# Kernel tuning notes

Hardware: AMD Instinct MI355X
Metric: run time of the kernel (lower is better)

## Reference

```python
import jax, jax.numpy as jnp
import numpy as np

N_NODES = 50000
N_EDGES = 800000
N_RELS = 32
D_IN = 64
D_OUT = 64


def setup_inputs() -> dict:
    key = jax.random.key(0)
    k_feat, k_w, k_src, k_dst, k_et = jax.random.split(key, 5)
    feat = jax.random.normal(k_feat, (N_NODES, D_IN), dtype=jnp.float32)
    weight = jax.random.normal(k_w, (N_RELS, D_IN, D_OUT), dtype=jnp.float32) * 0.05
    src = jax.random.randint(k_src, (N_EDGES,), 0, N_NODES, dtype=jnp.int32)
    dst = jax.random.randint(k_dst, (N_EDGES,), 0, N_NODES, dtype=jnp.int32)
    etypes = jax.random.randint(k_et, (N_EDGES,), 0, N_RELS, dtype=jnp.int32)
    # per-relation edge counts (unused by the unsorted math, kept for API fidelity)
    E_per_rel = jnp.bincount(etypes, length=N_RELS)
    return {"feat": feat, "weight": weight, "src": src, "dst": dst,
            "etypes": etypes, "E_per_rel": E_per_rel}


def reference(feat, weight, src, dst, etypes, E_per_rel):
    # out[d] = sum_{e: dst[e]==d} feat[src[e]] @ weight[etypes[e]]
    # Since the per-edge matmul is linear in feat, we first segment-sum the
    # gathered source features by (dst, etype), then apply each relation's
    # weight once. This avoids materializing an [E, D_IN, D_OUT] tensor.
    N = feat.shape[0]
    R, D_in, D_out = weight.shape
    gathered = feat[src]                                   # [E, D_in]
    seg = dst.astype(jnp.int32) * R + etypes.astype(jnp.int32)  # [E]
    per_node_rel = jax.ops.segment_sum(gathered, seg, num_segments=N * R)
    per_node_rel = per_node_rel.reshape(N, R, D_in)        # [N, R, D_in]
    out = jnp.einsum('nri,rio->no', per_node_rel, weight)  # [N, D_out]
    return out
```

## Files before the change

### kernel.cpp

```cpp
#include <hip/hip_runtime.h>
#include <hip/hip_bf16.h>

#define N_NODES 50000
#define N_EDGES 800000
#define N_RELS  32
#define D       64
#define TILE_M  128
#define NBKT    196
#define EPB     2048
#define NEBLK   ((N_EDGES + EPB - 1) / EPB)

typedef _Float16 half8 __attribute__((ext_vector_type(8)));
typedef float    f32x4 __attribute__((ext_vector_type(4)));

#define OFF_RELHIST 0u
#define OFF_BKTHIST 128u
#define OFF_RELCUR  1024u
#define OFF_BKTCUR  1152u
#define OFF_ROFF    1936u
#define OFF_TB      2080u
#define OFF_BKTOFF  2224u
#define OFF_DSTOFF  3072u
#define OFF_RELSRC  203776u
#define OFF_J2POS   3403776u
#define OFF_WT      6603776u
#define OFF_FEATH   6865920u
#define OFF_Y_FULL  13265920u
#define OFF_Y_BASE  6865920u
#define WS_FULL     115665920u
#define WS_BASE     109265920u

__global__ __launch_bounds__(256) void rgcn_edge_atomic(
    const float* __restrict__ feat, const float* __restrict__ weight,
    const int* __restrict__ src, const int* __restrict__ dst,
    const int* __restrict__ et, float* __restrict__ out, int nquads)
{
    const int tid  = blockIdx.x * blockDim.x + threadIdx.x;
    const int wave = tid >> 6, lane = tid & 63;
    const int grp = lane >> 4, lg = lane & 15;
    const int wave_stride = (gridDim.x * blockDim.x) >> 6;
    for (int q = wave; q < nquads; q += wave_stride) {
        const int e = q * 4 + grp;
        const int s = src[e], d = dst[e], r = et[e];
        const float* w = weight + (size_t)r * D * D + lg * 4;
        float ax = 0.f, ay = 0.f, az = 0.f, aw = 0.f;
        #pragma unroll
        for (int i4 = 0; i4 < D / 4; ++i4) {
            const float4 f  = *reinterpret_cast<const float4*>(feat + (size_t)s * D + i4 * 4);
            const float4 w0 = *reinterpret_cast<const float4*>(w + (i4 * 4 + 0) * D);
            const float4 w1 = *reinterpret_cast<const float4*>(w + (i4 * 4 + 1) * D);
            const float4 w2 = *reinterpret_cast<const float4*>(w + (i4 * 4 + 2) * D);
            const float4 w3 = *reinterpret_cast<const float4*>(w + (i4 * 4 + 3) * D);
            ax += f.x*w0.x; ay += f.x*w0.y; az += f.x*w0.z; aw += f.x*w0.w;
            ax += f.y*w1.x; ay += f.y*w1.y; az += f.y*w1.z; aw += f.y*w1.w;
            ax += f.z*w2.x; ay += f.z*w2.y; az += f.z*w2.z; aw += f.z*w2.w;
            ax += f.w*w3.x; ay += f.w*w3.y; az += f.w*w3.z; aw += f.w*w3.w;
        }
        float* orow = out + (size_t)d * D + lg * 4;
        atomicAdd(orow + 0, ax); atomicAdd(orow + 1, ay);
        atomicAdd(orow + 2, az); atomicAdd(orow + 3, aw);
    }
}

__global__ __launch_bounds__(256) void kPre(const float* __restrict__ w,
                                            _Float16* __restrict__ wT,
                                            const float* __restrict__ feat,
                                            _Float16* __restrict__ featH)
{
    const int t = threadIdx.x;
    if (blockIdx.x < N_RELS) {
        const int r = blockIdx.x;
        #pragma unroll
        for (int i = 0; i < 16; ++i) {
            int oidx = i * 256 + t;
            int o = oidx >> 6, k = oidx & 63;
            wT[(size_t)r * 4096 + oidx] = (_Float16)w[(size_t)r * 4096 + k * 64 + o];
        }
    } else {
        const int base = ((blockIdx.x - N_RELS) * 256 + t) * 8;
        if (base >= N_NODES * D) return;
        float4 f0 = *reinterpret_cast<const float4*>(feat + base);
        float4 f1 = *reinterpret_cast<const float4*>(feat + base + 4);
        half8 h;
        h[0]=(_Float16)f0.x; h[1]=(_Float16)f0.y; h[2]=(_Float16)f0.z; h[3]=(_Float16)f0.w;
        h[4]=(_Float16)f1.x; h[5]=(_Float16)f1.y; h[6]=(_Float16)f1.z; h[7]=(_Float16)f1.w;
        *reinterpret_cast<half8*>(featH + base) = h;
    }
}

__global__ __launch_bounds__(256) void kA_hist(const int* __restrict__ et,
                                               const int* __restrict__ dst,
                                               int* __restrict__ relhist,
                                               int* __restrict__ bkthist)
{
    __shared__ int lh[N_RELS];
    __shared__ int lb[NBKT];
    const int t = threadIdx.x;
    if (t < N_RELS) lh[t] = 0;
    if (t < NBKT)   lb[t] = 0;
    __syncthreads();
    const int base = blockIdx.x * EPB + t * 8;
    #pragma unroll
    for (int i = 0; i < 8; ++i) {
        int e = base + i;
        if (e < N_EDGES) {
            atomicAdd(&lh[et[e]], 1);
            atomicAdd(&lb[dst[e] >> 8], 1);
        }
    }
    __syncthreads();
    if (t < N_RELS && lh[t]) atomicAdd(&relhist[t], lh[t]);
    if (t < NBKT   && lb[t]) atomicAdd(&bkthist[t], lb[t]);
}

__global__ __launch_bounds__(256) void kB_scan(const int* __restrict__ relhist,
                                               const int* __restrict__ bkthist,
                                               int* __restrict__ roff,
                                               int* __restrict__ relcur,
                                               int* __restrict__ tb,
                                               int* __restrict__ bktoff,
                                               int* __restrict__ bktcur,
                                               int* __restrict__ dst_off)
{
    __shared__ int s[256];
    const int t = threadIdx.x;
    int v = (t < N_RELS) ? relhist[t] : 0;
    s[t] = v; __syncthreads();
    #pragma unroll
    for (int off = 1; off < 32; off <<= 1) {
        int u = (t >= off && t < N_RELS) ? s[t - off] : 0;
        __syncthreads(); s[t] += u; __syncthreads();
    }
    if (t < N_RELS) { int ex = s[t] - v; roff[t] = ex; relcur[t] = ex; }
    if (t == N_RELS - 1) roff[N_RELS] = s[t];
    __syncthreads();
    int w = (v + TILE_M - 1) / TILE_M;
    s[t] = (t < N_RELS) ? w : 0; __syncthreads();
    #pragma unroll
    for (int off = 1; off < 32; off <<= 1) {
        int u = (t >= off && t < N_RELS) ? s[t - off] : 0;
        __syncthreads(); s[t] += u; __syncthreads();
    }
    if (t < N_RELS) tb[t] = s[t] - w;
    if (t == N_RELS - 1) tb[N_RELS] = s[t];
    __syncthreads();
    int v2 = (t < NBKT) ? bkthist[t] : 0;
    s[t] = v2; __syncthreads();
    #pragma unroll
    for (int off = 1; off < 256; off <<= 1) {
        int u = (t >= off) ? s[t - off] : 0;
        __syncthreads(); s[t] += u; __syncthreads();
    }
    if (t < NBKT) { int ex = s[t] - v2; bktoff[t] = ex; bktcur[t] = ex; }
    if (t == NBKT - 1) bktoff[NBKT] = s[t];
    if (t == 0) dst_off[N_NODES] = N_EDGES;
}

__global__ __launch_bounds__(256) void kC_scatter(const int* __restrict__ src,
                                                  const int* __restrict__ dst,
                                                  const int* __restrict__ et,
                                                  int* __restrict__ relcur,
                                                  int* __restrict__ bktcur,
                                                  int* __restrict__ relsrc,
                                                  int* __restrict__ bucketed)
{
    __shared__ int lh[N_RELS],  lbase[N_RELS];
    __shared__ int lb[NBKT],    lbase2[NBKT];
    const int t = threadIdx.x;
    if (t < N_RELS) lh[t] = 0;
    if (t < NBKT)   lb[t] = 0;
    __syncthreads();
    const int base = blockIdx.x * EPB + t * 8;
    int r_[8], b_[8], s_[8], d_[8], sl[8], sl2[8];
    #pragma unroll
    for (int i = 0; i < 8; ++i) {
        int e = base + i;
        if (e < N_EDGES) {
            r_[i] = et[e]; s_[i] = src[e]; d_[i] = dst[e];
            b_[i] = d_[i] >> 8;
            sl[i]  = atomicAdd(&lh[r_[i]], 1);
            sl2[i] = atomicAdd(&lb[b_[i]], 1);
        }
    }
    __syncthreads();
    if (t < N_RELS && lh[t]) lbase[t]  = atomicAdd(&relcur[t], lh[t]);
    if (t < NBKT   && lb[t]) lbase2[t] = atomicAdd(&bktcur[t], lb[t]);
    __syncthreads();
    #pragma unroll
    for (int i = 0; i < 8; ++i) {
        int e = base + i;
        if (e < N_EDGES) {
            int j = lbase[r_[i]] + sl[i];
            relsrc[j] = s_[i];
            bucketed[lbase2[b_[i]] + sl2[i]] = ((d_[i] & 255) << 20) | j;
        }
    }
}

__global__ __launch_bounds__(256) void kD_csr(const int* __restrict__ bucketed,
                                              const int* __restrict__ bktoff,
                                              int* __restrict__ j2pos,
                                              int* __restrict__ dst_off)
{
    __shared__ int hist[256];
    __shared__ int s[256];
    const int b = blockIdx.x, t = threadIdx.x;
    const int lo = bktoff[b], hi = bktoff[b + 1];
    hist[t] = 0; __syncthreads();
    for (int p = lo + t; p < hi; p += 256)
        atomicAdd(&hist[bucketed[p] >> 20], 1);
    __syncthreads();
    int v = hist[t];
    s[t] = v; __syncthreads();
    #pragma unroll
    for (int off = 1; off < 256; off <<= 1) {
        int u = (t >= off) ? s[t - off] : 0;
        __syncthreads(); s[t] += u; __syncthreads();
    }
    int ex = lo + s[t] - v;
    int n = b * 256 + t;
    if (n < N_NODES) dst_off[n] = ex;
    hist[t] = ex;
    __syncthreads();
    for (int p = lo + t; p < hi; p += 256) {
        int key = bucketed[p];
        int pos = atomicAdd(&hist[key >> 20], 1);
        j2pos[key & 0xFFFFF] = pos;
    }
}

template <bool USE_H>
__global__ __launch_bounds__(256) void k4_gemm(const float* __restrict__ feat,
                                               const _Float16* __restrict__ featH,
                                               const _Float16* __restrict__ wT,
                                               const int* __restrict__ relsrc,
                                               const int* __restrict__ j2pos,
                                               const int* __restrict__ roff,
                                               const int* __restrict__ tb,
                                               _Float16* __restrict__ Y)
{
    __shared__ _Float16 aT[TILE_M * 64];
    __shared__ _Float16 wL[64 * 64];
    __shared__ int      ypos[TILE_M];
    const int b = blockIdx.x, t = threadIdx.x;

    int r = -1, ti = 0, t0 = 0;
    #pragma unroll
    for (int q = 0; q < N_RELS; ++q) {
        int t1 = tb[q + 1];
        if (b >= t0 && b < t1) { r = q; ti = b - t0; }
        t0 = t1;
    }
    if (r < 0) return;
    const int segend  = roff[r + 1];
    const int rowbase = roff[r] + ti * TILE_M;

    if (t < TILE_M) {
        const int j = rowbase + t;
        const bool ok = (j < segend);
        const int sidx = ok ? relsrc[j] : 0;
        ypos[t] = ok ? j2pos[j] : 0;
        if (USE_H) {
            const half8* hrow = reinterpret_cast<const half8*>(featH + (size_t)sidx * 64);
            #pragma unroll
            for (int c = 0; c < 4; ++c) {
                half8 h0 = hrow[c * 2 + 0];
                half8 h1 = hrow[c * 2 + 1];
                int base = t * 128 + c * 32;
                int a0 = (base)      ^ ((t & 7) << 4);
                int a1 = (base + 16) ^ ((t & 7) << 4);
                *reinterpret_cast<half8*>(reinterpret_cast<char*>(aT) + a0) = h0;
                *reinterpret_cast<half8*>(reinterpret_cast<char*>(aT) + a1) = h1;
            }
        } else {
            const float4* frow = reinterpret_cast<const float4*>(feat + (size_t)sidx * 64);
            #pragma unroll
            for (int c = 0; c < 4; ++c) {
                float4 f0 = frow[c*4+0], f1 = frow[c*4+1], f2 = frow[c*4+2], f3 = frow[c*4+3];
                half8 h0, h1;
                h0[0]=(_Float16)f0.x; h0[1]=(_Float16)f0.y; h0[2]=(_Float16)f0.z; h0[3]=(_Float16)f0.w;
                h0[4]=(_Float16)f1.x; h0[5]=(_Float16)f1.y; h0[6]=(_Float16)f1.z; h0[7]=(_Float16)f1.w;
                h1[0]=(_Float16)f2.x; h1[1]=(_Float16)f2.y; h1[2]=(_Float16)f2.z; h1[3]=(_Float16)f2.w;
                h1[4]=(_Float16)f3.x; h1[5]=(_Float16)f3.y; h1[6]=(_Float16)f3.z; h1[7]=(_Float16)f3.w;
                int base = t * 128 + c * 32;
                int a0 = (base)      ^ ((t & 7) << 4);
                int a1 = (base + 16) ^ ((t & 7) << 4);
                *reinterpret_cast<half8*>(reinterpret_cast<char*>(aT) + a0) = h0;
                *reinterpret_cast<half8*>(reinterpret_cast<char*>(aT) + a1) = h1;
            }
        }
    } else {
        const _Float16* wsrc = wT + (size_t)r * 4096;
        const int tt = t - 128;
        #pragma unroll
        for (int it = 0; it < 4; ++it) {
            int L8 = it * 128 + tt;
            int o = L8 >> 3, kcol = (L8 & 7) * 8;
            int baddr = (o * 128 + kcol * 2) ^ ((o & 7) << 4);
            *reinterpret_cast<half8*>(reinterpret_cast<char*>(wL) + baddr) =
                *reinterpret_cast<const half8*>(wsrc + L8 * 8);
        }
    }
    __syncthreads();

    const int wid = t >> 6, l = t & 63;
    const int lrow = l & 15, lkb = l >> 4;
    f32x4 acc[2][4] = {};
    #pragma unroll
    for (int ks = 0; ks < 2; ++ks) {
        half8 af[2], bfr[4];
        #pragma unroll
        for (int rt = 0; rt < 2; ++rt) {
            int row = wid * 32 + rt * 16 + lrow;
            int baddr = (row * 128 + ks * 64 + lkb * 16) ^ ((row & 7) << 4);
            af[rt] = *reinterpret_cast<const half8*>(reinterpret_cast<const char*>(aT) + baddr);
        }
        #pragma unroll
        for (int ct = 0; ct < 4; ++ct) {
            int n = ct * 16 + lrow;
            int baddr = (n * 128 + ks * 64 + lkb * 16) ^ ((n & 7) << 4);
            bfr[ct] = *reinterpret_cast<const half8*>(reinterpret_cast<const char*>(wL) + baddr);
        }
        #pragma unroll
        for (int rt = 0; rt < 2; ++rt)
            #pragma unroll
            for (int ct = 0; ct < 4; ++ct)
                acc[rt][ct] = __builtin_amdgcn_mfma_f32_16x16x32_f16(af[rt], bfr[ct], acc[rt][ct], 0, 0, 0);
    }
    #pragma unroll
    for (int rt = 0; rt < 2; ++rt) {
        int lrow0 = wid * 32 + rt * 16 + (l >> 4) * 4;
        #pragma unroll
        for (int reg = 0; reg < 4; ++reg) {
            int lr = lrow0 + reg;
            if (rowbase + lr < segend) {
                size_t yrow = (size_t)ypos[lr] * 64;
                #pragma unroll
                for (int ct = 0; ct < 4; ++ct)
                    Y[yrow + ct * 16 + lrow] = (_Float16)acc[rt][ct][reg];
            }
        }
    }
}

__global__ __launch_bounds__(256) void k5_reduce(const _Float16* __restrict__ Y,
                                                 const int* __restrict__ dst_off,
                                                 float* __restrict__ out)
{
    const int wid = threadIdx.x >> 6, l = threadIdx.x & 63;
    const int n = blockIdx.x * 4 + wid;
    if (n >= N_NODES) return;
    const int p0 = dst_off[n], p1 = dst_off[n + 1];
    float acc = 0.f;
    int p = p0;
    for (; p + 4 <= p1; p += 4) {
        acc += (float)Y[(size_t)(p+0) * 64 + l] + (float)Y[(size_t)(p+1) * 64 + l]
             + (float)Y[(size_t)(p+2) * 64 + l] + (float)Y[(size_t)(p+3) * 64 + l];
    }
    for (; p < p1; ++p)
        acc += (float)Y[(size_t)p * 64 + l];
    out[(size_t)n * 64 + l] = acc;
}

extern "C" void kernel_launch(void* const* d_in, const int* in_sizes, int n_in,
                              void* d_out, int out_size, void* d_ws, size_t ws_size,
                              hipStream_t stream) {
    const float* feat   = (const float*)d_in[0];
    const float* weight = (const float*)d_in[1];
    const int*   src    = (const int*)d_in[2];
    const int*   dst    = (const int*)d_in[3];
    const int*   et     = (const int*)d_in[4];
    float*       out    = (float*)d_out;

    if (ws_size < (size_t)WS_BASE) {
        hipMemsetAsync(d_out, 0, (size_t)out_size * sizeof(float), stream);
        hipLaunchKernelGGL(rgcn_edge_atomic, dim3(4096), dim3(256), 0, stream,
                           feat, weight, src, dst, et, out, N_EDGES / 4);
        return;
    }
    const bool use_h = (ws_size >= (size_t)WS_FULL);

    char* ws = (char*)d_ws;
    int*       relhist  = (int*)(ws + OFF_RELHIST);
    int*       bkthist  = (int*)(ws + OFF_BKTHIST);
    int*       relcur   = (int*)(ws + OFF_RELCUR);
    int*       bktcur   = (int*)(ws + OFF_BKTCUR);
    int*       roff     = (int*)(ws + OFF_ROFF);
    int*       tb       = (int*)(ws + OFF_TB);
    int*       bktoff   = (int*)(ws + OFF_BKTOFF);
    int*       dst_off  = (int*)(ws + OFF_DSTOFF);
    int*       relsrc   = (int*)(ws + OFF_RELSRC);
    int*       j2pos    = (int*)(ws + OFF_J2POS);
    _Float16*  wT       = (_Float16*)(ws + OFF_WT);
    _Float16*  featH    = (_Float16*)(ws + OFF_FEATH);
    _Float16*  Y        = (_Float16*)(ws + (use_h ? OFF_Y_FULL : OFF_Y_BASE));
    int*       bucketed = (int*)Y;

    hipMemsetAsync(ws, 0, 912, stream);

    const int pre_blocks = use_h ? (N_RELS + (N_NODES * D / 8 + 255) / 256) : N_RELS;
    hipLaunchKernelGGL(kPre,       dim3(pre_blocks), dim3(256), 0, stream, weight, wT, feat, featH);
    hipLaunchKernelGGL(kA_hist,    dim3(NEBLK),  dim3(256), 0, stream, et, dst, relhist, bkthist);
    hipLaunchKernelGGL(kB_scan,    dim3(1),      dim3(256), 0, stream, relhist, bkthist, roff, relcur, tb, bktoff, bktcur, dst_off);
    hipLaunchKernelGGL(kC_scatter, dim3(NEBLK),  dim3(256), 0, stream, src, dst, et, relcur, bktcur, relsrc, bucketed);
    hipLaunchKernelGGL(kD_csr,     dim3(NBKT),   dim3(256), 0, stream, bucketed, bktoff, j2pos, dst_off);
    const int max_tiles = N_EDGES / TILE_M + N_RELS;
    if (use_h)
        hipLaunchKernelGGL((k4_gemm<true>),  dim3(max_tiles), dim3(256), 0, stream, feat, featH, wT, relsrc, j2pos, roff, tb, Y);
    else
        hipLaunchKernelGGL((k4_gemm<false>), dim3(max_tiles), dim3(256), 0, stream, feat, featH, wT, relsrc, j2pos, roff, tb, Y);
    hipLaunchKernelGGL(k5_reduce,  dim3((N_NODES + 3) / 4), dim3(256), 0, stream, Y, dst_off, out);
}
```

Before: 119.5 us.

## Fuse histogram with preprocessing, vectorize reduce, split gemm tile loads across all threads

Measured after the change: 130.4 us. +9.2%, slower.

```diff
diff --git a/kernel.cpp b/kernel.cpp
--- a/kernel.cpp
+++ b/kernel.cpp
@@ -7,8 +7,10 @@
 #define D       64
 #define TILE_M  128
 #define NBKT    196
-#define EPB     2048
+#define EPB     1024
+#define EPT     4
 #define NEBLK   ((N_EDGES + EPB - 1) / EPB)
+#define FEATH_BLKS ((N_NODES * D / 8 + 255) / 256)
 
 typedef _Float16 half8 __attribute__((ext_vector_type(8)));
 typedef float    f32x4 __attribute__((ext_vector_type(4)));
@@ -62,14 +64,41 @@
     }
 }
 
-__global__ __launch_bounds__(256) void kPre(const float* __restrict__ w,
-                                            _Float16* __restrict__ wT,
-                                            const float* __restrict__ feat,
-                                            _Float16* __restrict__ featH)
-{
-    const int t = threadIdx.x;
-    if (blockIdx.x < N_RELS) {
-        const int r = blockIdx.x;
+__global__ __launch_bounds__(256) void kZ_zero(int* __restrict__ h)
+{
+    if (threadIdx.x < 228) h[threadIdx.x] = 0;
+}
+
+__global__ __launch_bounds__(256) void kA_fused(const int* __restrict__ et,
+                                                const int* __restrict__ dst,
+                                                int* __restrict__ relhist,
+                                                int* __restrict__ bkthist,
+                                                const float* __restrict__ w,
+                                                _Float16* __restrict__ wT,
+                                                const float* __restrict__ feat,
+                                                _Float16* __restrict__ featH)
+{
+    __shared__ int lh[N_RELS];
+    __shared__ int lb[NBKT];
+    const int t = threadIdx.x, b = blockIdx.x;
+    if (b < NEBLK) {
+        if (t < N_RELS) lh[t] = 0;
+        if (t < NBKT)   lb[t] = 0;
+        __syncthreads();
+        const int base = b * EPB + t * EPT;
+        #pragma unroll
+        for (int i = 0; i < EPT; ++i) {
+            int e = base + i;
+            if (e < N_EDGES) {
+                atomicAdd(&lh[et[e]], 1);
+                atomicAdd(&lb[dst[e] >> 8], 1);
+            }
+        }
+        __syncthreads();
+        if (t < N_RELS && lh[t]) atomicAdd(&relhist[t], lh[t]);
+        if (t < NBKT   && lb[t]) atomicAdd(&bkthist[t], lb[t]);
+    } else if (b < NEBLK + N_RELS) {
+        const int r = b - NEBLK;
         #pragma unroll
         for (int i = 0; i < 16; ++i) {
             int oidx = i * 256 + t;
@@ -77,40 +106,15 @@
             wT[(size_t)r * 4096 + oidx] = (_Float16)w[(size_t)r * 4096 + k * 64 + o];
         }
     } else {
-        const int base = ((blockIdx.x - N_RELS) * 256 + t) * 8;
-        if (base >= N_NODES * D) return;
-        float4 f0 = *reinterpret_cast<const float4*>(feat + base);
-        float4 f1 = *reinterpret_cast<const float4*>(feat + base + 4);
+        const int base2 = ((b - NEBLK - N_RELS) * 256 + t) * 8;
+        if (base2 >= N_NODES * D) return;
+        float4 f0 = *reinterpret_cast<const float4*>(feat + base2);
+        float4 f1 = *reinterpret_cast<const float4*>(feat + base2 + 4);
         half8 h;
         h[0]=(_Float16)f0.x; h[1]=(_Float16)f0.y; h[2]=(_Float16)f0.z; h[3]=(_Float16)f0.w;
         h[4]=(_Float16)f1.x; h[5]=(_Float16)f1.y; h[6]=(_Float16)f1.z; h[7]=(_Float16)f1.w;
-        *reinterpret_cast<half8*>(featH + base) = h;
-    }
-}
-
-__global__ __launch_bounds__(256) void kA_hist(const int* __restrict__ et,
-                                               const int* __restrict__ dst,
-                                               int* __restrict__ relhist,
-                                               int* __restrict__ bkthist)
-{
-    __shared__ int lh[N_RELS];
-    __shared__ int lb[NBKT];
-    const int t = threadIdx.x;
-    if (t < N_RELS) lh[t] = 0;
-    if (t < NBKT)   lb[t] = 0;
-    __syncthreads();
-    const int base = blockIdx.x * EPB + t * 8;
-    #pragma unroll
-    for (int i = 0; i < 8; ++i) {
-        int e = base + i;
-        if (e < N_EDGES) {
-            atomicAdd(&lh[et[e]], 1);
-            atomicAdd(&lb[dst[e] >> 8], 1);
-        }
-    }
-    __syncthreads();
-    if (t < N_RELS && lh[t]) atomicAdd(&relhist[t], lh[t]);
-    if (t < NBKT   && lb[t]) atomicAdd(&bkthist[t], lb[t]);
+        *reinterpret_cast<half8*>(featH + base2) = h;
+    }
 }
 
 __global__ __launch_bounds__(256) void kB_scan(const int* __restrict__ relhist,
@@ -170,10 +174,10 @@
     if (t < N_RELS) lh[t] = 0;
     if (t < NBKT)   lb[t] = 0;
     __syncthreads();
-    const int base = blockIdx.x * EPB + t * 8;
-    int r_[8], b_[8], s_[8], d_[8], sl[8], sl2[8];
-    #pragma unroll
-    for (int i = 0; i < 8; ++i) {
+    const int base = blockIdx.x * EPB + t * EPT;
+    int r_[EPT], b_[EPT], s_[EPT], d_[EPT], sl[EPT], sl2[EPT];
+    #pragma unroll
+    for (int i = 0; i < EPT; ++i) {
         int e = base + i;
         if (e < N_EDGES) {
             r_[i] = et[e]; s_[i] = src[e]; d_[i] = dst[e];
@@ -187,7 +191,7 @@
     if (t < NBKT   && lb[t]) lbase2[t] = atomicAdd(&bktcur[t], lb[t]);
     __syncthreads();
     #pragma unroll
-    for (int i = 0; i < 8; ++i) {
+    for (int i = 0; i < EPT; ++i) {
         int e = base + i;
         if (e < N_EDGES) {
             int j = lbase[r_[i]] + sl[i];
@@ -255,46 +259,44 @@
     const int segend  = roff[r + 1];
     const int rowbase = roff[r] + ti * TILE_M;
 
-    if (t < TILE_M) {
-        const int j = rowbase + t;
+    {
+        const int row = t & 127, hh = t >> 7;
+        const int j = rowbase + row;
         const bool ok = (j < segend);
         const int sidx = ok ? relsrc[j] : 0;
-        ypos[t] = ok ? j2pos[j] : 0;
+        if (hh == 0) ypos[row] = ok ? j2pos[j] : 0;
+        const int sw = (row & 7) << 4;
         if (USE_H) {
             const half8* hrow = reinterpret_cast<const half8*>(featH + (size_t)sidx * 64);
             #pragma unroll
-            for (int c = 0; c < 4; ++c) {
+            for (int cc = 0; cc < 2; ++cc) {
+                int c = hh * 2 + cc;
                 half8 h0 = hrow[c * 2 + 0];
                 half8 h1 = hrow[c * 2 + 1];
-                int base = t * 128 + c * 32;
-                int a0 = (base)      ^ ((t & 7) << 4);
-                int a1 = (base + 16) ^ ((t & 7) << 4);
-                *reinterpret_cast<half8*>(reinterpret_cast<char*>(aT) + a0) = h0;
-                *reinterpret_cast<half8*>(reinterpret_cast<char*>(aT) + a1) = h1;
+                int base = row * 128 + c * 32;
+                *reinterpret_cast<half8*>(reinterpret_cast<char*>(aT) + ((base)      ^ sw)) = h0;
+                *reinterpret_cast<half8*>(reinterpret_cast<char*>(aT) + ((base + 16) ^ sw)) = h1;
             }
         } else {
             const float4* frow = reinterpret_cast<const float4*>(feat + (size_t)sidx * 64);
             #pragma unroll
-            for (int c = 0; c < 4; ++c) {
+            for (int cc = 0; cc < 2; ++cc) {
+                int c = hh * 2 + cc;
                 float4 f0 = frow[c*4+0], f1 = frow[c*4+1], f2 = frow[c*4+2], f3 = frow[c*4+3];
                 half8 h0, h1;
                 h0[0]=(_Float16)f0.x; h0[1]=(_Float16)f0.y; h0[2]=(_Float16)f0.z; h0[3]=(_Float16)f0.w;
                 h0[4]=(_Float16)f1.x; h0[5]=(_Float16)f1.y; h0[6]=(_Float16)f1.z; h0[7]=(_Float16)f1.w;
                 h1[0]=(_Float16)f2.x; h1[1]=(_Float16)f2.y; h1[2]=(_Float16)f2.z; h1[3]=(_Float16)f2.w;
                 h1[4]=(_Float16)f3.x; h1[5]=(_Float16)f3.y; h1[6]=(_Float16)f3.z; h1[7]=(_Float16)f3.w;
-                int base = t * 128 + c * 32;
-                int a0 = (base)      ^ ((t & 7) << 4);
-                int a1 = (base + 16) ^ ((t & 7) << 4);
-                *reinterpret_cast<half8*>(reinterpret_cast<char*>(aT) + a0) = h0;
-                *reinterpret_cast<half8*>(reinterpret_cast<char*>(aT) + a1) = h1;
+                int base = row * 128 + c * 32;
+                *reinterpret_cast<half8*>(reinterpret_cast<char*>(aT) + ((base)      ^ sw)) = h0;
+                *reinterpret_cast<half8*>(reinterpret_cast<char*>(aT) + ((base + 16) ^ sw)) = h1;
             }
         }
-    } else {
         const _Float16* wsrc = wT + (size_t)r * 4096;
-        const int tt = t - 128;
-        #pragma unroll
-        for (int it = 0; it < 4; ++it) {
-            int L8 = it * 128 + tt;
+        #pragma unroll
+        for (int it = 0; it < 2; ++it) {
+            int L8 = it * 256 + t;
             int o = L8 >> 3, kcol = (L8 & 7) * 8;
             int baddr = (o * 128 + kcol * 2) ^ ((o & 7) << 4);
             *reinterpret_cast<half8*>(reinterpret_cast<char*>(wL) + baddr) =
@@ -351,15 +353,29 @@
     const int n = blockIdx.x * 4 + wid;
     if (n >= N_NODES) return;
     const int p0 = dst_off[n], p1 = dst_off[n + 1];
-    float acc = 0.f;
-    int p = p0;
-    for (; p + 4 <= p1; p += 4) {
-        acc += (float)Y[(size_t)(p+0) * 64 + l] + (float)Y[(size_t)(p+1) * 64 + l]
-             + (float)Y[(size_t)(p+2) * 64 + l] + (float)Y[(size_t)(p+3) * 64 + l];
-    }
-    for (; p < p1; ++p)
-        acc += (float)Y[(size_t)p * 64 + l];
-    out[(size_t)n * 64 + l] = acc;
+    const int rg = l >> 3;
+    const int cg = l & 7;
+    float a[8] = {0,0,0,0,0,0,0,0};
+    for (int p = p0; p < p1; p += 8) {
+        int row = p + rg;
+        if (row < p1) {
+            half8 v = *reinterpret_cast<const half8*>(Y + (size_t)row * 64 + cg * 8);
+            #pragma unroll
+            for (int i = 0; i < 8; ++i) a[i] += (float)v[i];
+        }
+    }
+    #pragma unroll
+    for (int m = 8; m < 64; m <<= 1)
+        #pragma unroll
+        for (int i = 0; i < 8; ++i)
+            a[i] += __shfl_xor(a[i], m, 64);
+    if (rg == 0) {
+        float* orow = out + (size_t)n * 64 + cg * 8;
+        f32x4 v0 = {a[0], a[1], a[2], a[3]};
+        f32x4 v1 = {a[4], a[5], a[6], a[7]};
+        *reinterpret_cast<f32x4*>(orow)     = v0;
+        *reinterpret_cast<f32x4*>(orow + 4) = v1;
+    }
 }
 
 extern "C" void kernel_launch(void* const* d_in, const int* in_sizes, int n_in,
@@ -396,18 +412,17 @@
     _Float16*  Y        = (_Float16*)(ws + (use_h ? OFF_Y_FULL : OFF_Y_BASE));
     int*       bucketed = (int*)Y;
 
-    hipMemsetAsync(ws, 0, 912, stream);
-
-    const int pre_blocks = use_h ? (N_RELS + (N_NODES * D / 8 + 255) / 256) : N_RELS;
-    hipLaunchKernelGGL(kPre,       dim3(pre_blocks), dim3(256), 0, stream, weight, wT, feat, featH);
-    hipLaunchKernelGGL(kA_hist,    dim3(NEBLK),  dim3(256), 0, stream, et, dst, relhist, bkthist);
-    hipLaunchKernelGGL(kB_scan,    dim3(1),      dim3(256), 0, stream, relhist, bkthist, roff, relcur, tb, bktoff, bktcur, dst_off);
-    hipLaunchKernelGGL(kC_scatter, dim3(NEBLK),  dim3(256), 0, stream, src, dst, et, relcur, bktcur, relsrc, bucketed);
-    hipLaunchKernelGGL(kD_csr,     dim3(NBKT),   dim3(256), 0, stream, bucketed, bktoff, j2pos, dst_off);
+    hipLaunchKernelGGL(kZ_zero,   dim3(1), dim3(256), 0, stream, (int*)ws);
+    const int ka_blocks = NEBLK + N_RELS + (use_h ? FEATH_BLKS : 0);
+    hipLaunchKernelGGL(kA_fused,  dim3(ka_blocks), dim3(256), 0, stream,
+                       et, dst, relhist, bkthist, weight, wT, feat, featH);
+    hipLaunchKernelGGL(kB_scan,   dim3(1),     dim3(256), 0, stream, relhist, bkthist, roff, relcur, tb, bktoff, bktcur, dst_off);
+    hipLaunchKernelGGL(kC_scatter,dim3(NEBLK), dim3(256), 0, stream, src, dst, et, relcur, bktcur, relsrc, bucketed);
+    hipLaunchKernelGGL(kD_csr,    dim3(NBKT),  dim3(256), 0, stream, bucketed, bktoff, j2pos, dst_off);
     const int max_tiles = N_EDGES / TILE_M + N_RELS;
     if (use_h)
         hipLaunchKernelGGL((k4_gemm<true>),  dim3(max_tiles), dim3(256), 0, stream, feat, featH, wT, relsrc, j2pos, roff, tb, Y);
     else
         hipLaunchKernelGGL((k4_gemm<false>), dim3(max_tiles), dim3(256), 0, stream, feat, featH, wT, relsrc, j2pos, roff, tb, Y);
-    hipLaunchKernelGGL(k5_reduce,  dim3((N_NODES + 3) / 4), dim3(256), 0, stream, Y, dst_off, out);
-}
+    hipLaunchKernelGGL(k5_reduce, dim3((N_NODES + 3) / 4), dim3(256), 0, stream, Y, dst_off, out);
+}
```
